# Performance work log

Measured on AMD Instinct MI355X. Metric: run time of the kernel, lower is better.

## Reference

```python
import jax, jax.numpy as jnp
import numpy as np

B, N, C, H = 2, 1024, 768, 12
D = C // H
SCALE = D ** -0.5


def setup_inputs() -> dict:
    key = jax.random.key(0)
    ks = jax.random.split(key, 6)
    s = 1.0 / np.sqrt(C)
    return {
        "x": jax.random.normal(ks[0], (B, N, C), jnp.float32),
        "Wqkv": jax.random.normal(ks[1], (3 * C, C), jnp.float32) * s,   # qkv_bias=False
        "Wa": jax.random.normal(ks[2], (H, C), jnp.float32) * s,        # selective gate Linear(dim, H)
        "ba": jnp.zeros((H,), jnp.float32),
        "Wproj": jax.random.normal(ks[3], (C, C), jnp.float32) * s,
        "bproj": jnp.zeros((C,), jnp.float32),
    }


def _silu_shifted(z):
    # silu(x) + 0.5, L2-normalized over head dim (silunorm=True)
    r = jax.nn.silu(z) + 0.5
    return r / jnp.linalg.norm(r, axis=-1, keepdims=True)


def _forward(x, Wqkv, Wa, ba, Wproj, bproj):
    qkv = (x @ Wqkv.T).reshape(B, N, 3, H, D).transpose(2, 0, 3, 1, 4)  # [3,B,H,N,D]
    q = _silu_shifted(qkv[0])
    k = _silu_shifted(qkv[1])
    v = qkv[2]

    # selective forget gates: a = 1 - sigmoid(Linear(x)); torch.tensor(...) detaches -> stop_gradient
    a = jax.lax.stop_gradient(1.0 - jax.nn.sigmoid(x @ Wa.T + ba)).transpose(0, 2, 1)  # [B,H,N]
    # drop first token's gate, prepend 1 (as in the module)
    a = jnp.concatenate([jnp.ones_like(a[..., :1]), a[..., 1:]], axis=-1)

    # Causal_Mask_Selective(log(a)):
    #   A_for[i,j]  = prod_{t=j..i-1} a[t]   (j <= i)
    #   A_back[i,j] = prod_{t=i+1..j} a[t]   (j >= i)
    #   M = A_for + A_back - I
    c = jnp.cumsum(jnp.log(a), axis=-1)
    c = jnp.concatenate([jnp.zeros_like(c[..., :1]), c], axis=-1)  # [B,H,N+1], c[m] = sum log a[0..m-1]
    tri = jnp.tril(jnp.ones((N, N), bool))
    d_for = c[..., :N, None] - c[..., None, :N]      # c[i]-c[j]
    d_back = c[..., None, 1:] - c[..., 1:, None]     # c[j+1]-c[i+1]
    A_for = jnp.where(tri, jnp.exp(jnp.where(tri, d_for, 0.0)), 0.0)
    A_back = jnp.where(tri.T, jnp.exp(jnp.where(tri.T, d_back, 0.0)), 0.0)
    M = A_for + A_back - jnp.eye(N, dtype=x.dtype)

    attn = jnp.einsum('bhid,bhjd->bhij', q, k) * SCALE * M
    attn = attn / (attn.sum(axis=-1, keepdims=True) + 1e-6)  # sum-normalization, NOT softmax
    out = jnp.einsum('bhij,bhjd->bhid', attn, v).transpose(0, 2, 1, 3).reshape(B, N, C)
    return out @ Wproj.T + bproj


def reference(x, Wqkv, Wa, ba, Wproj, bproj):
    return _forward(x, Wqkv, Wa, ba, Wproj, bproj)
```

## Files before the change

### kernel.cpp

```cpp
#include <hip/hip_runtime.h>
#include <hip/hip_bf16.h>

#define BB 2
#define NN 1024
#define CC 768
#define HH 12
#define DD 64
#define SCALE_F 0.125f

typedef __attribute__((ext_vector_type(8))) __bf16 bf16x8;
typedef __attribute__((ext_vector_type(8))) unsigned short u16x8;
typedef __attribute__((ext_vector_type(4))) unsigned short u16x4;
typedef __attribute__((ext_vector_type(4))) float f32x4;

static __device__ __forceinline__ bf16x8 as_bf16x8(u16x8 v) {
  return __builtin_bit_cast(bf16x8, v);
}
static __device__ __forceinline__ unsigned short bf16u(float f) {
  __hip_bfloat16 h = __float2bfloat16(f);
  return __builtin_bit_cast(unsigned short, h);
}
static __device__ __forceinline__ float bf2f(unsigned short u) {
  unsigned int x = ((unsigned int)u) << 16;
  return __builtin_bit_cast(float, x);
}
static __device__ __forceinline__ void gload16(const void* g, void* l) {
  __builtin_amdgcn_global_load_lds(
      (const __attribute__((address_space(1))) unsigned int*)g,
      (__attribute__((address_space(3))) unsigned int*)l, 16, 0, 0);
}

__global__ __launch_bounds__(256) void pack3_bf16(
    const float* __restrict__ s0, unsigned short* __restrict__ d0, int n0,
    const float* __restrict__ s1, unsigned short* __restrict__ d1, int n1,
    const float* __restrict__ s2, unsigned short* __restrict__ d2, int n2) {
  int i = blockIdx.x * 256 + threadIdx.x;
  const float* s;
  unsigned short* d;
  if (i < n0) {
    s = s0; d = d0;
  } else if (i < n0 + n1) {
    i -= n0; s = s1; d = d1;
  } else {
    i -= n0 + n1;
    if (i >= n2) return;
    s = s2; d = d2;
  }
  float4 v = ((const float4*)s)[i];
  u16x4 u = {bf16u(v.x), bf16u(v.y), bf16u(v.z), bf16u(v.w)};
  *(u16x4*)&d[i * 4] = u;
}

template <int BM, int BN, bool BF16OUT>
__global__ __launch_bounds__(256) void gemm_mfma(
    const unsigned short* __restrict__ A, const unsigned short* __restrict__ W,
    const float* __restrict__ bias, void* __restrict__ outv,
    int M, int Nc, int K) {
  __shared__ unsigned short As[BM * 64];
  __shared__ unsigned short Ws[BN * 64];
  constexpr int FM = BM / 32, FN = BN / 32;
  const int row0 = blockIdx.y * BM;
  const int col0 = blockIdx.x * BN;
  const int t = threadIdx.x;
  const int w = t >> 6, lane = t & 63;
  const int lrow = lane & 15, lgrp = lane >> 4;
  const int wr = w >> 1, wc = w & 1;

  f32x4 acc[FM][FN] = {};

  for (int k0 = 0; k0 < K; k0 += 64) {
#pragma unroll
    for (int i = 0; i < BM * 8 / 256; i++) {
      int idx = i * 256 + t;
      int row = idx >> 3, sl = (idx & 7) ^ (row & 7);
      gload16(A + (size_t)(row0 + row) * K + k0 + sl * 8, &As[idx * 8]);
    }
#pragma unroll
    for (int i = 0; i < BN * 8 / 256; i++) {
      int idx = i * 256 + t;
      int row = idx >> 3, sl = (idx & 7) ^ (row & 7);
      gload16(W + (size_t)(col0 + row) * K + k0 + sl * 8, &Ws[idx * 8]);
    }
    __syncthreads();

    bf16x8 af[FM][2], bf[FN][2];
#pragma unroll
    for (int m = 0; m < FM; m++) {
      int row = wr * (BM / 2) + m * 16 + lrow;
      const u16x8* p = (const u16x8*)&As[row * 64];
#pragma unroll
      for (int hk = 0; hk < 2; hk++)
        af[m][hk] = as_bf16x8(p[(hk * 4 + lgrp) ^ (row & 7)]);
    }
#pragma unroll
    for (int n = 0; n < FN; n++) {
      int row = wc * (BN / 2) + n * 16 + lrow;
      const u16x8* p = (const u16x8*)&Ws[row * 64];
#pragma unroll
      for (int hk = 0; hk < 2; hk++)
        bf[n][hk] = as_bf16x8(p[(hk * 4 + lgrp) ^ (row & 7)]);
    }
#pragma unroll
    for (int m = 0; m < FM; m++)
#pragma unroll
      for (int n = 0; n < FN; n++) {
        acc[m][n] = __builtin_amdgcn_mfma_f32_16x16x32_bf16(
            af[m][0], bf[n][0], acc[m][n], 0, 0, 0);
        acc[m][n] = __builtin_amdgcn_mfma_f32_16x16x32_bf16(
            af[m][1], bf[n][1], acc[m][n], 0, 0, 0);
      }
    __syncthreads();
  }

#pragma unroll
  for (int n = 0; n < FN; n++) {
    int col = col0 + wc * (BN / 2) + n * 16 + lrow;
    float bb = (!BF16OUT && bias) ? bias[col] : 0.f;
#pragma unroll
    for (int m = 0; m < FM; m++) {
      int rbase = row0 + wr * (BM / 2) + m * 16 + lgrp * 4;
#pragma unroll
      for (int r = 0; r < 4; r++) {
        float v = acc[m][n][r] + bb;
        if (BF16OUT)
          ((unsigned short*)outv)[(size_t)(rbase + r) * Nc + col] = bf16u(v);
        else
          ((float*)outv)[(size_t)(rbase + r) * Nc + col] = v;
      }
    }
  }
}

__global__ __launch_bounds__(256) void qkv_pack(
    const unsigned short* __restrict__ qkvb, unsigned short* __restrict__ qp,
    unsigned short* __restrict__ kp, unsigned short* __restrict__ vt) {
  __shared__ unsigned short tile[64][65];
  if (blockIdx.x < 12288) {
    const int wid = (blockIdx.x * 256 + threadIdx.x) >> 6;
    const int lane = threadIdx.x & 63;
    int s = wid & 1;
    int rest = wid >> 1;
    int h = rest % HH;
    int n = (rest / HH) % NN;
    int b = rest / (HH * NN);
    float z = bf2f(qkvb[(((size_t)(b * NN + n) * 3 + s) * CC) + h * DD + lane]);
    float sig = 1.f / (1.f + __expf(-z));
    float r = z * sig + 0.5f;
    float ss = r * r;
#pragma unroll
    for (int off = 32; off >= 1; off >>= 1) ss += __shfl_xor(ss, off, 64);
    r *= rsqrtf(ss);
    unsigned short* dst = s ? kp : qp;
    dst[((size_t)(b * HH + h) * NN + n) * DD + lane] = bf16u(r);
  } else {
    const int blk = blockIdx.x - 12288;
    const int nt = blk & 15;
    const int bh = blk >> 4;
    const int b = bh / HH, h = bh % HH;
    const int n0 = nt * 64;
    const int t = threadIdx.x;
#pragma unroll
    for (int rep = 0; rep < 16; rep++) {
      int idx = rep * 256 + t;
      int nl = idx >> 6, d = idx & 63;
      tile[d][nl] =
          qkvb[((size_t)(b * NN + n0 + nl) * 3 + 2) * CC + h * DD + d];
    }
    __syncthreads();
#pragma unroll
    for (int rep = 0; rep < 16; rep++) {
      int idx = rep * 256 + t;
      int d = idx >> 6, nl = idx & 63;
      vt[((size_t)bh * DD + d) * NN + n0 + nl] = tile[d][nl];
    }
  }
}

__global__ __launch_bounds__(256) void gate_kernel(
    const float* __restrict__ x, const float* __restrict__ Wa,
    const float* __restrict__ ba, float* __restrict__ loga) {
  __shared__ float was[HH][CC];
  for (int i = threadIdx.x; i < HH * CC; i += 256) was[i / CC][i % CC] = Wa[i];
  __syncthreads();
  const int w = threadIdx.x >> 6, lane = threadIdx.x & 63;
  const int row = blockIdx.x * 4 + w;
  const int b = row >> 10, n = row & 1023;
  const float* xr = x + (size_t)row * CC;
  float xf[12];
#pragma unroll
  for (int j = 0; j < 12; j++) xf[j] = xr[lane + 64 * j];
  float myacc = 0.f;
#pragma unroll
  for (int h = 0; h < HH; h++) {
    float a = 0.f;
#pragma unroll
    for (int j = 0; j < 12; j++) a += xf[j] * was[h][lane + 64 * j];
#pragma unroll
    for (int off = 32; off >= 1; off >>= 1) a += __shfl_xor(a, off, 64);
    if (lane == h) myacc = a;
  }
  if (lane < HH) {
    float acc = myacc + ba[lane];
    float a = 1.f - 1.f / (1.f + __expf(-acc));
    float la = (n == 0) ? 0.f : log2f(a);
    loga[(b * HH + lane) * NN + n] = la;
  }
}

__global__ __launch_bounds__(64) void scan_kernel(
    const float* __restrict__ loga, float* __restrict__ c) {
  const int bh = blockIdx.x;
  const int lane = threadIdx.x;
  const float4* s4 = (const float4*)(loga + (size_t)bh * NN + lane * 16);
  float v[16];
#pragma unroll
  for (int q = 0; q < 4; q++) {
    float4 t = s4[q];
    v[q * 4 + 0] = t.x; v[q * 4 + 1] = t.y;
    v[q * 4 + 2] = t.z; v[q * 4 + 3] = t.w;
  }
  float run = 0.f;
#pragma unroll
  for (int e = 0; e < 16; e++) { run += v[e]; v[e] = run; }
  float tot = run;
#pragma unroll
  for (int off = 1; off < 64; off <<= 1) {
    float nb = __shfl_up(tot, off, 64);
    if (lane >= off) tot += nb;
  }
  float excl = tot - run;
  float* dst = c + (size_t)bh * (NN + 1);
  if (lane == 0) dst[0] = 0.f;
#pragma unroll
  for (int e = 0; e < 16; e++) dst[1 + lane * 16 + e] = v[e] + excl;
}

__global__ __launch_bounds__(256) void attn_mfma(
    const unsigned short* __restrict__ qp, const unsigned short* __restrict__ kp,
    const unsigned short* __restrict__ vt, const float* __restrict__ cbuf,
    unsigned short* __restrict__ attnout) {
  __shared__ unsigned short Ks[2][64 * 64];
  __shared__ unsigned short Vs[2][64 * 64];
  __shared__ unsigned short Aw[4][16 * 64];
  __shared__ float Cw[2][64][17];
  __shared__ float Rw[2][64][5];

  const int qt2 = blockIdx.x & 31;
  const int bh = blockIdx.x >> 5;
  const int b = bh / HH, h = bh % HH;
  const int qrow0 = qt2 * 32;
  const int w = threadIdx.x >> 6;
  const int lane = threadIdx.x & 63;
  const int lrow = lane & 15;
  const int lgrp = lane >> 4;
  const int wq = w & 1;
  const int js = w >> 1;

  bf16x8 qaf[2];
  {
    const u16x8* qrow_p = (const u16x8*)(qp +
        ((size_t)bh * NN + qrow0 + wq * 16 + lrow) * DD);
#pragma unroll
    for (int hk = 0; hk < 2; hk++) qaf[hk] = as_bf16x8(qrow_p[hk * 4 + lgrp]);
  }

  const float* cbh = cbuf + (size_t)bh * (NN + 1);
  float ci[4], ci1[4];
  const int ibase = qrow0 + wq * 16 + lgrp * 4;
#pragma unroll
  for (int r = 0; r < 4; r++) {
    ci[r] = cbh[ibase + r];
    ci1[r] = cbh[ibase + r + 1];
  }

  f32x4 oacc[4] = {};
  float rs[4] = {0.f, 0.f, 0.f, 0.f};

  unsigned short* ksf = &Ks[0][0];
  unsigned short* vsf = &Vs[0][0];

  for (int t = 0; t < 8; t++) {
#pragma unroll
    for (int rep = 0; rep < 4; rep++) {
      int idx = rep * 256 + threadIdx.x;
      int buf = idx >> 9, row = (idx >> 3) & 63;
      int sl = (idx & 7) ^ (row & 7);
      int j0s = (buf * 8 + t) * 64;
      gload16(kp + ((size_t)bh * NN + j0s + row) * DD + sl * 8, ksf + idx * 8);
      gload16(vt + ((size_t)bh * DD + row) * NN + j0s + sl * 8, vsf + idx * 8);
    }
    __syncthreads();

    const int j0 = (js * 8 + t) * 64;

#pragma unroll
    for (int ct = 0; ct < 4; ct++) {
      const int jl = ct * 16 + lrow;
      const int j = j0 + jl;
      f32x4 s = {};
      const u16x8* krow_p = (const u16x8*)&Ks[js][jl * 64];
#pragma unroll
      for (int hk = 0; hk < 2; hk++) {
        bf16x8 kf = as_bf16x8(krow_p[(hk * 4 + lgrp) ^ (jl & 7)]);
        s = __builtin_amdgcn_mfma_f32_16x16x32_bf16(qaf[hk], kf, s, 0, 0, 0);
      }
      const float cj = cbh[j], cj1 = cbh[j + 1];
#pragma unroll
      for (int r = 0; r < 4; r++) {
        const int gi = ibase + r;
        float m = (gi > j) ? exp2f(ci[r] - cj)
                 : (gi < j) ? exp2f(cj1 - ci1[r]) : 1.0f;
        float av = s[r] * SCALE_F * m;
        rs[r] += av;
        int rowa = lgrp * 4 + r;
        Aw[w][rowa * 64 + (jl ^ ((rowa & 7) << 3))] = bf16u(av);
      }
    }

#pragma unroll
    for (int jh = 0; jh < 2; jh++) {
      const u16x8* arow_p = (const u16x8*)&Aw[w][lrow * 64];
      bf16x8 af = as_bf16x8(arow_p[(jh * 4 + lgrp) ^ (lrow & 7)]);
#pragma unroll
      for (int dt = 0; dt < 4; dt++) {
        const int dd = dt * 16 + lrow;
        const u16x8* vrow_p = (const u16x8*)&Vs[js][dd * 64];
        bf16x8 vf = as_bf16x8(vrow_p[(jh * 4 + lgrp) ^ (dd & 7)]);
        oacc[dt] =
            __builtin_amdgcn_mfma_f32_16x16x32_bf16(af, vf, oacc[dt], 0, 0, 0);
      }
    }
    __syncthreads();
  }

#pragma unroll
  for (int r = 0; r < 4; r++) {
#pragma unroll
    for (int off = 1; off <= 8; off <<= 1) rs[r] += __shfl_xor(rs[r], off, 64);
  }

  if (w >= 2) {
#pragma unroll
    for (int dt = 0; dt < 4; dt++)
#pragma unroll
      for (int r = 0; r < 4; r++) Cw[w - 2][lane][dt * 4 + r] = oacc[dt][r];
#pragma unroll
    for (int r = 0; r < 4; r++) Rw[w - 2][lane][r] = rs[r];
  }
  __syncthreads();
  if (w < 2) {
#pragma unroll
    for (int r = 0; r < 4; r++) {
      rs[r] += Rw[w][lane][r];
      rs[r] = 1.f / (rs[r] + 1e-6f);
    }
#pragma unroll
    for (int dt = 0; dt < 4; dt++) {
#pragma unroll
      for (int r = 0; r < 4; r++) {
        const int gi = ibase + r;
        float val = (oacc[dt][r] + Cw[w][lane][dt * 4 + r]) * rs[r];
        attnout[((size_t)b * NN + gi) * CC + h * DD + dt * 16 + lrow] =
            bf16u(val);
      }
    }
  }
}

extern "C" void kernel_launch(void* const* d_in, const int* in_sizes, int n_in,
                              void* d_out, int out_size, void* d_ws,
                              size_t ws_size, hipStream_t stream) {
  const float* x = (const float*)d_in[0];
  const float* Wqkv = (const float*)d_in[1];
  const float* Wa = (const float*)d_in[2];
  const float* ba = (const float*)d_in[3];
  const float* Wproj = (const float*)d_in[4];
  const float* bproj = (const float*)d_in[5];
  float* out = (float*)d_out;

  unsigned short* qkvb = (unsigned short*)d_ws;
  float* loga = (float*)(qkvb + (size_t)BB * NN * 3 * CC);
  float* cbuf = loga + (size_t)BB * HH * NN;
  unsigned short* qp = (unsigned short*)(cbuf + (size_t)BB * HH * (NN + 1));
  unsigned short* kp = qp + (size_t)BB * HH * NN * DD;
  unsigned short* vt = kp + (size_t)BB * HH * NN * DD;
  unsigned short* xb = vt + (size_t)BB * HH * NN * DD;
  unsigned short* wqkvb = xb + (size_t)BB * NN * CC;
  unsigned short* wprojb = wqkvb + (size_t)3 * CC * CC;
  unsigned short* attnoutb = qkvb;

  {
    int n0 = BB * NN * CC / 4, n1 = 3 * CC * CC / 4, n2 = CC * CC / 4;
    pack3_bf16<<<(n0 + n1 + n2 + 255) / 256, 256, 0, stream>>>(
        x, xb, n0, Wqkv, wqkvb, n1, Wproj, wprojb, n2);
  }
  {
    dim3 grid(3 * CC / 128, BB * NN / 128);
    gemm_mfma<128, 128, true><<<grid, 256, 0, stream>>>(
        xb, wqkvb, nullptr, qkvb, BB * NN, 3 * CC, CC);
  }
  qkv_pack<<<12672, 256, 0, stream>>>(qkvb, qp, kp, vt);
  gate_kernel<<<BB * NN / 4, 256, 0, stream>>>(x, Wa, ba, loga);
  scan_kernel<<<BB * HH, 64, 0, stream>>>(loga, cbuf);
  attn_mfma<<<BB * HH * (NN / 32), 256, 0, stream>>>(qp, kp, vt, cbuf,
                                                     attnoutb);
  {
    dim3 grid(CC / 64, BB * NN / 64);
    gemm_mfma<64, 64, false><<<grid, 256, 0, stream>>>(
        attnoutb, wprojb, bproj, out, BB * NN, CC, CC);
  }
}
```

Before: 154.8 us.

## Merge gate/pack and scan/qkv-pack kernels, double-buffer GEMM LDS, shrink QKV tile

The gate projection now runs inside the bf16 packing kernel, and the prefix-scan runs inside the qkv repack kernel as extra blocks. This cuts the launch count from seven to five. The GEMM now double-buffers its LDS tiles so the next K-slice's global-to-LDS loads overlap the MFMA work on the current slice. The QKV GEMM tile shrinks from 128x128 to 64x128, doubling the block count for better CU occupancy, at the cost of more LDS per block and more redundant weight loads.

```diff
diff --git a/kernel.cpp b/kernel.cpp
--- a/kernel.cpp
+++ b/kernel.cpp
@@ -30,25 +30,58 @@
       (__attribute__((address_space(3))) unsigned int*)l, 16, 0, 0);
 }
 
-__global__ __launch_bounds__(256) void pack3_bf16(
-    const float* __restrict__ s0, unsigned short* __restrict__ d0, int n0,
-    const float* __restrict__ s1, unsigned short* __restrict__ d1, int n1,
-    const float* __restrict__ s2, unsigned short* __restrict__ d2, int n2) {
-  int i = blockIdx.x * 256 + threadIdx.x;
-  const float* s;
-  unsigned short* d;
-  if (i < n0) {
-    s = s0; d = d0;
-  } else if (i < n0 + n1) {
-    i -= n0; s = s1; d = d1;
+__global__ __launch_bounds__(256) void packgate(
+    const float* __restrict__ x, const float* __restrict__ Wa,
+    const float* __restrict__ ba, float* __restrict__ loga,
+    unsigned short* __restrict__ xb, int n0,
+    const float* __restrict__ Wqkv, unsigned short* __restrict__ wqkvb, int n1,
+    const float* __restrict__ Wproj, unsigned short* __restrict__ wprojb,
+    int n2) {
+  __shared__ float was[HH][CC];
+  if (blockIdx.x < 512) {
+    for (int i = threadIdx.x; i < HH * CC; i += 256)
+      was[i / CC][i % CC] = Wa[i];
+    __syncthreads();
+    const int w = threadIdx.x >> 6, lane = threadIdx.x & 63;
+    const int row = blockIdx.x * 4 + w;
+    const int b = row >> 10, n = row & 1023;
+    const float* xr = x + (size_t)row * CC;
+    float xf[12];
+#pragma unroll
+    for (int j = 0; j < 12; j++) xf[j] = xr[lane + 64 * j];
+    float myacc = 0.f;
+#pragma unroll
+    for (int h = 0; h < HH; h++) {
+      float a = 0.f;
+#pragma unroll
+      for (int j = 0; j < 12; j++) a += xf[j] * was[h][lane + 64 * j];
+#pragma unroll
+      for (int off = 32; off >= 1; off >>= 1) a += __shfl_xor(a, off, 64);
+      if (lane == h) myacc = a;
+    }
+    if (lane < HH) {
+      float acc = myacc + ba[lane];
+      float a = 1.f - 1.f / (1.f + __expf(-acc));
+      float la = (n == 0) ? 0.f : log2f(a);
+      loga[(b * HH + lane) * NN + n] = la;
+    }
   } else {
-    i -= n0 + n1;
-    if (i >= n2) return;
-    s = s2; d = d2;
-  }
-  float4 v = ((const float4*)s)[i];
-  u16x4 u = {bf16u(v.x), bf16u(v.y), bf16u(v.z), bf16u(v.w)};
-  *(u16x4*)&d[i * 4] = u;
+    int i = (blockIdx.x - 512) * 256 + threadIdx.x;
+    const float* s;
+    unsigned short* d;
+    if (i < n0) {
+      s = x; d = xb;
+    } else if (i < n0 + n1) {
+      i -= n0; s = Wqkv; d = wqkvb;
+    } else {
+      i -= n0 + n1;
+      if (i >= n2) return;
+      s = Wproj; d = wprojb;
+    }
+    float4 v = ((const float4*)s)[i];
+    u16x4 u = {bf16u(v.x), bf16u(v.y), bf16u(v.z), bf16u(v.w)};
+    *(u16x4*)&d[i * 4] = u;
+  }
 }
 
 template <int BM, int BN, bool BF16OUT>
@@ -56,8 +89,8 @@
     const unsigned short* __restrict__ A, const unsigned short* __restrict__ W,
     const float* __restrict__ bias, void* __restrict__ outv,
     int M, int Nc, int K) {
-  __shared__ unsigned short As[BM * 64];
-  __shared__ unsigned short Ws[BN * 64];
+  __shared__ unsigned short As[2][BM * 64];
+  __shared__ unsigned short Ws[2][BN * 64];
   constexpr int FM = BM / 32, FN = BN / 32;
   const int row0 = blockIdx.y * BM;
   const int col0 = blockIdx.x * BN;
@@ -68,26 +101,34 @@
 
   f32x4 acc[FM][FN] = {};
 
-  for (int k0 = 0; k0 < K; k0 += 64) {
+  auto STAGE = [&](int buf, int k0) {
 #pragma unroll
     for (int i = 0; i < BM * 8 / 256; i++) {
       int idx = i * 256 + t;
       int row = idx >> 3, sl = (idx & 7) ^ (row & 7);
-      gload16(A + (size_t)(row0 + row) * K + k0 + sl * 8, &As[idx * 8]);
+      gload16(A + (size_t)(row0 + row) * K + k0 + sl * 8, &As[buf][idx * 8]);
     }
 #pragma unroll
     for (int i = 0; i < BN * 8 / 256; i++) {
       int idx = i * 256 + t;
       int row = idx >> 3, sl = (idx & 7) ^ (row & 7);
-      gload16(W + (size_t)(col0 + row) * K + k0 + sl * 8, &Ws[idx * 8]);
-    }
-    __syncthreads();
+      gload16(W + (size_t)(col0 + row) * K + k0 + sl * 8, &Ws[buf][idx * 8]);
+    }
+  };
+
+  const int NT = K / 64;
+  STAGE(0, 0);
+  __syncthreads();
+
+  for (int tt = 0; tt < NT; tt++) {
+    const int cur = tt & 1;
+    if (tt + 1 < NT) STAGE(cur ^ 1, (tt + 1) * 64);
 
     bf16x8 af[FM][2], bf[FN][2];
 #pragma unroll
     for (int m = 0; m < FM; m++) {
       int row = wr * (BM / 2) + m * 16 + lrow;
-      const u16x8* p = (const u16x8*)&As[row * 64];
+      const u16x8* p = (const u16x8*)&As[cur][row * 64];
 #pragma unroll
       for (int hk = 0; hk < 2; hk++)
         af[m][hk] = as_bf16x8(p[(hk * 4 + lgrp) ^ (row & 7)]);
@@ -95,7 +136,7 @@
 #pragma unroll
     for (int n = 0; n < FN; n++) {
       int row = wc * (BN / 2) + n * 16 + lrow;
-      const u16x8* p = (const u16x8*)&Ws[row * 64];
+      const u16x8* p = (const u16x8*)&Ws[cur][row * 64];
 #pragma unroll
       for (int hk = 0; hk < 2; hk++)
         bf[n][hk] = as_bf16x8(p[(hk * 4 + lgrp) ^ (row & 7)]);
@@ -131,9 +172,10 @@
   }
 }
 
-__global__ __launch_bounds__(256) void qkv_pack(
+__global__ __launch_bounds__(256) void packscan(
     const unsigned short* __restrict__ qkvb, unsigned short* __restrict__ qp,
-    unsigned short* __restrict__ kp, unsigned short* __restrict__ vt) {
+    unsigned short* __restrict__ kp, unsigned short* __restrict__ vt,
+    const float* __restrict__ loga, float* __restrict__ c) {
   __shared__ unsigned short tile[64][65];
   if (blockIdx.x < 12288) {
     const int wid = (blockIdx.x * 256 + threadIdx.x) >> 6;
@@ -152,7 +194,7 @@
     r *= rsqrtf(ss);
     unsigned short* dst = s ? kp : qp;
     dst[((size_t)(b * HH + h) * NN + n) * DD + lane] = bf16u(r);
-  } else {
+  } else if (blockIdx.x < 12672) {
     const int blk = blockIdx.x - 12288;
     const int nt = blk & 15;
     const int bh = blk >> 4;
@@ -173,66 +215,32 @@
       int d = idx >> 6, nl = idx & 63;
       vt[((size_t)bh * DD + d) * NN + n0 + nl] = tile[d][nl];
     }
-  }
-}
-
-__global__ __launch_bounds__(256) void gate_kernel(
-    const float* __restrict__ x, const float* __restrict__ Wa,
-    const float* __restrict__ ba, float* __restrict__ loga) {
-  __shared__ float was[HH][CC];
-  for (int i = threadIdx.x; i < HH * CC; i += 256) was[i / CC][i % CC] = Wa[i];
-  __syncthreads();
-  const int w = threadIdx.x >> 6, lane = threadIdx.x & 63;
-  const int row = blockIdx.x * 4 + w;
-  const int b = row >> 10, n = row & 1023;
-  const float* xr = x + (size_t)row * CC;
-  float xf[12];
-#pragma unroll
-  for (int j = 0; j < 12; j++) xf[j] = xr[lane + 64 * j];
-  float myacc = 0.f;
-#pragma unroll
-  for (int h = 0; h < HH; h++) {
-    float a = 0.f;
-#pragma unroll
-    for (int j = 0; j < 12; j++) a += xf[j] * was[h][lane + 64 * j];
-#pragma unroll
-    for (int off = 32; off >= 1; off >>= 1) a += __shfl_xor(a, off, 64);
-    if (lane == h) myacc = a;
-  }
-  if (lane < HH) {
-    float acc = myacc + ba[lane];
-    float a = 1.f - 1.f / (1.f + __expf(-acc));
-    float la = (n == 0) ? 0.f : log2f(a);
-    loga[(b * HH + lane) * NN + n] = la;
-  }
-}
-
-__global__ __launch_bounds__(64) void scan_kernel(
-    const float* __restrict__ loga, float* __restrict__ c) {
-  const int bh = blockIdx.x;
-  const int lane = threadIdx.x;
-  const float4* s4 = (const float4*)(loga + (size_t)bh * NN + lane * 16);
-  float v[16];
-#pragma unroll
-  for (int q = 0; q < 4; q++) {
-    float4 t = s4[q];
-    v[q * 4 + 0] = t.x; v[q * 4 + 1] = t.y;
-    v[q * 4 + 2] = t.z; v[q * 4 + 3] = t.w;
-  }
-  float run = 0.f;
-#pragma unroll
-  for (int e = 0; e < 16; e++) { run += v[e]; v[e] = run; }
-  float tot = run;
-#pragma unroll
-  for (int off = 1; off < 64; off <<= 1) {
-    float nb = __shfl_up(tot, off, 64);
-    if (lane >= off) tot += nb;
-  }
-  float excl = tot - run;
-  float* dst = c + (size_t)bh * (NN + 1);
-  if (lane == 0) dst[0] = 0.f;
-#pragma unroll
-  for (int e = 0; e < 16; e++) dst[1 + lane * 16 + e] = v[e] + excl;
+  } else if (threadIdx.x < 64) {
+    const int bh = blockIdx.x - 12672;
+    const int lane = threadIdx.x;
+    const float4* s4 = (const float4*)(loga + (size_t)bh * NN + lane * 16);
+    float v[16];
+#pragma unroll
+    for (int q = 0; q < 4; q++) {
+      float4 tv = s4[q];
+      v[q * 4 + 0] = tv.x; v[q * 4 + 1] = tv.y;
+      v[q * 4 + 2] = tv.z; v[q * 4 + 3] = tv.w;
+    }
+    float run = 0.f;
+#pragma unroll
+    for (int e = 0; e < 16; e++) { run += v[e]; v[e] = run; }
+    float tot = run;
+#pragma unroll
+    for (int off = 1; off < 64; off <<= 1) {
+      float nb = __shfl_up(tot, off, 64);
+      if (lane >= off) tot += nb;
+    }
+    float excl = tot - run;
+    float* dst = c + (size_t)bh * (NN + 1);
+    if (lane == 0) dst[0] = 0.f;
+#pragma unroll
+    for (int e = 0; e < 16; e++) dst[1 + lane * 16 + e] = v[e] + excl;
+  }
 }
 
 __global__ __launch_bounds__(256) void attn_mfma(
@@ -389,19 +397,16 @@
   unsigned short* wprojb = wqkvb + (size_t)3 * CC * CC;
   unsigned short* attnoutb = qkvb;
 
+  const int n0 = BB * NN * CC / 4, n1 = 3 * CC * CC / 4, n2 = CC * CC / 4;
+
+  packgate<<<512 + (n0 + n1 + n2 + 255) / 256, 256, 0, stream>>>(
+      x, Wa, ba, loga, xb, n0, Wqkv, wqkvb, n1, Wproj, wprojb, n2);
   {
-    int n0 = BB * NN * CC / 4, n1 = 3 * CC * CC / 4, n2 = CC * CC / 4;
-    pack3_bf16<<<(n0 + n1 + n2 + 255) / 256, 256, 0, stream>>>(
-        x, xb, n0, Wqkv, wqkvb, n1, Wproj, wprojb, n2);
-  }
-  {
-    dim3 grid(3 * CC / 128, BB * NN / 128);
-    gemm_mfma<128, 128, true><<<grid, 256, 0, stream>>>(
+    dim3 grid(3 * CC / 128, BB * NN / 64);
+    gemm_mfma<64, 128, true><<<grid, 256, 0, stream>>>(
         xb, wqkvb, nullptr, qkvb, BB * NN, 3 * CC, CC);
   }
-  qkv_pack<<<12672, 256, 0, stream>>>(qkvb, qp, kp, vt);
-  gate_kernel<<<BB * NN / 4, 256, 0, stream>>>(x, Wa, ba, loga);
-  scan_kernel<<<BB * HH, 64, 0, stream>>>(loga, cbuf);
+  packscan<<<12696, 256, 0, stream>>>(qkvb, qp, kp, vt, loga, cbuf);
   attn_mfma<<<BB * HH * (NN / 32), 256, 0, stream>>>(qp, kp, vt, cbuf,
                                                      attnoutb);
   {
```

New measurement: 146.3 us. 1.06x faster.
